# Optimization experiments

Measured on AMD Instinct MI355X. Metric: run time of the kernel, lower is better.

## Reference

```python
import jax, jax.numpy as jnp
import numpy as np

N, E, F_IN, EDGE_DIM, H, C, NUM_RELS = 20000, 160000, 64, 8, 4, 128, 4


def setup_inputs() -> dict:
    key = jax.random.key(0)
    ks = jax.random.split(key, 20)
    def rn(k, shape, s=0.05):
        return jax.random.normal(k, shape, jnp.float32) * s
    return {
        "x": rn(ks[0], (N, F_IN), 1.0),
        "edge_index": jax.random.randint(ks[1], (2, E), 0, N, dtype=jnp.int32),
        "edge_features": rn(ks[2], (E, EDGE_DIM), 1.0),
        "W1": rn(ks[3], (F_IN, H * C)), "a_src1": rn(ks[4], (H, C)), "a_dst1": rn(ks[5], (H, C)),
        "We1": rn(ks[6], (EDGE_DIM, H * C)), "a_e1": rn(ks[7], (H, C)), "b1": jnp.zeros((H * C,), jnp.float32),
        "W2": rn(ks[8], (H * C, H * C)), "a_src2": rn(ks[9], (H, C)), "a_dst2": rn(ks[10], (H, C)),
        "We2": rn(ks[11], (EDGE_DIM, H * C)), "a_e2": rn(ks[12], (H, C)), "b2": jnp.zeros((H * C,), jnp.float32),
        "Wd1": rn(ks[13], (2 * H * C, 256)), "bd1": jnp.zeros((256,), jnp.float32),
        "Wd2": rn(ks[14], (256, NUM_RELS)), "bd2": jnp.zeros((NUM_RELS,), jnp.float32),
    }


def _add_self_loops(ei, ea, n):
    # PyG add_self_loops with fill_value='mean': self-loop edge_attr is the
    # mean of incoming edge_attr per destination node (0 if no incoming edges).
    dst = ei[1]
    s = jax.ops.segment_sum(ea, dst, num_segments=n)
    cnt = jax.ops.segment_sum(jnp.ones((ea.shape[0], 1), ea.dtype), dst, num_segments=n)
    mean = s / jnp.maximum(cnt, 1.0)
    loop = jnp.arange(n, dtype=ei.dtype)
    ei2 = jnp.concatenate([ei, jnp.stack([loop, loop])], axis=1)
    ea2 = jnp.concatenate([ea, mean], axis=0)
    return ei2, ea2


def _gat_conv(x, ei, ea, W, a_s, a_d, We, a_e, b, n):
    ei, ea = _add_self_loops(ei, ea, n)
    src, dst = ei[0], ei[1]
    xp = (x @ W).reshape(n, H, C)                      # [N,H,C]
    alpha_s = jnp.einsum('nhc,hc->nh', xp, a_s)        # [N,H]
    alpha_d = jnp.einsum('nhc,hc->nh', xp, a_d)        # [N,H]
    ep = (ea @ We).reshape(-1, H, C)                   # [E',H,C]
    alpha_e = jnp.einsum('ehc,hc->eh', ep, a_e)        # [E',H]
    alpha = alpha_s[src] + alpha_d[dst] + alpha_e
    alpha = jax.nn.leaky_relu(alpha, 0.2)
    # segment softmax over edges sharing a destination node
    m = jax.ops.segment_max(alpha, dst, num_segments=n)
    ex = jnp.exp(alpha - m[dst])
    den = jax.ops.segment_sum(ex, dst, num_segments=n)
    w = ex / den[dst]                                   # [E',H]
    out = jax.ops.segment_sum(xp[src] * w[..., None], dst, num_segments=n)  # [N,H,C]
    return out.reshape(n, H * C) + b


def reference(x, edge_index, edge_features, W1, a_src1, a_dst1, We1, a_e1, b1,
              W2, a_src2, a_dst2, We2, a_e2, b2, Wd1, bd1, Wd2, bd2):
    n = x.shape[0]
    z = jax.nn.elu(_gat_conv(x, edge_index, edge_features, W1, a_src1, a_dst1, We1, a_e1, b1, n))
    z = jax.nn.elu(_gat_conv(z, edge_index, edge_features, W2, a_src2, a_dst2, We2, a_e2, b2, n))
    src, dst = edge_index[0], edge_index[1]
    rel = jnp.concatenate([z[src], z[dst]], axis=1)     # [E, 2*512]
    h = rel @ Wd1 + bd1                                 # dropout is identity at inference
    return jax.nn.sigmoid(h @ Wd2 + bd2)
```

## Files before the change

kernel.cpp:

```cpp
#include <hip/hip_runtime.h>
#include <hip/hip_bf16.h>
#include <math.h>

#define N_NODES 20000
#define N_EDGES 160000
#define FIN 64
#define EDGE_DIM 8
#define H_HEADS 4
#define C_CH 128
#define HC 512
#define NUM_RELS 4
#define E_TOT (N_EDGES + N_NODES)
#define E_PAD 320256

typedef __bf16 bf16x8 __attribute__((ext_vector_type(8)));
typedef __bf16 bf16x4 __attribute__((ext_vector_type(4)));
typedef float f32x4 __attribute__((ext_vector_type(4)));
typedef unsigned short u16x8 __attribute__((ext_vector_type(8)));

#define NZ4 ((N_NODES + E_PAD) / 4)
#define NM4 (E_PAD / 4)
__global__ void k_fill(int4* __restrict__ zbase, int4* __restrict__ mbase) {
    int tid = blockIdx.x * 256 + threadIdx.x;
    if (tid < NZ4) {
        zbase[tid] = make_int4(0, 0, 0, 0);
    } else if (tid < NZ4 + NM4) {
        mbase[tid - NZ4] = make_int4(-1, -1, -1, -1);
    }
}

#define NX4 (N_NODES * FIN / 4)
#define W1T (HC * FIN)
#define W2T (HC * HC)
#define NCVTB ((NX4 + W1T + W2T) / 256)
__global__ void k_prep_all(const float* __restrict__ x, __bf16* __restrict__ xb,
                           const float* __restrict__ W1, __bf16* __restrict__ Wt1,
                           const float* __restrict__ W2, __bf16* __restrict__ Wt2,
                           const float* __restrict__ We1, const float* __restrict__ ae1,
                           const float* __restrict__ We2, const float* __restrict__ ae2,
                           float* __restrict__ q1, float* __restrict__ q2,
                           const float* __restrict__ Wd1, const float* __restrict__ Wd2,
                           const float* __restrict__ bd1, const float* __restrict__ bd2,
                           float* __restrict__ M, float* __restrict__ cvec,
                           const float* __restrict__ as1, const float* __restrict__ ad1,
                           float* __restrict__ w1as, float* __restrict__ w1ad) {
    int bid = blockIdx.x;
    if (bid < NCVTB) {
        int tid = bid * 256 + threadIdx.x;
        if (tid < NX4) {
            float4 v = *(const float4*)(x + (size_t)tid * 4);
            __bf16 o[4] = {(__bf16)v.x, (__bf16)v.y, (__bf16)v.z, (__bf16)v.w};
            *(ushort2*)(xb + (size_t)tid * 4) = *(ushort2*)o;
            *(ushort2*)(xb + (size_t)tid * 4 + 2) = *(ushort2*)(o + 2);
        } else if (tid < NX4 + W1T) {
            int t = tid - NX4;
            int n = t / FIN, k = t % FIN;
            Wt1[n * FIN + k] = (__bf16)W1[(size_t)k * HC + n];
        } else {
            int t = tid - NX4 - W1T;
            int n = t >> 9, k = t & 511;
            Wt2[n * HC + k] = (__bf16)W2[(size_t)k * HC + n];
        }
        return;
    }
    int pb = bid - NCVTB;
    if (pb == 16) {
        int t = threadIdx.x;
        if (t >= 64) return;
        const float* We = (t < 32) ? We1 : We2;
        const float* ae = (t < 32) ? ae1 : ae2;
        float* q = (t < 32) ? q1 : q2;
        int i = t & 31, h = i >> 3, d = i & 7;
        float s = 0.f;
        for (int c = 0; c < 128; ++c) s += We[d * 512 + h * 128 + c] * ae[h * 128 + c];
        q[i] = s;
    } else if (pb == 17 || pb == 18) {
        int t = threadIdx.x;
        int h = t >> 6, k = t & 63;
        const float* av = (pb == 17) ? as1 : ad1;
        float* outp = (pb == 17) ? w1as : w1ad;
        float s = 0.f;
        for (int c = 0; c < 128; ++c) s += W1[(size_t)k * HC + h * 128 + c] * av[h * 128 + c];
        outp[h * 64 + k] = s;
    } else {
        int tid = pb * 256 + threadIdx.x;
        int i = tid >> 2, r = tid & 3;
        float s = 0.f;
        for (int k = 0; k < 256; ++k) s += Wd1[i * 256 + k] * Wd2[k * 4 + r];
        M[tid] = s;
        if (tid < 4) {
            float c = 0.f;
            for (int k = 0; k < 256; ++k) c += bd1[k] * Wd2[k * 4 + tid];
            cvec[tid] = c + bd2[tid];
        }
    }
}

#define LDP 40
__global__ __launch_bounds__(256)
void k_gemm_bf16(const __bf16* __restrict__ A, const __bf16* __restrict__ Bt,
                 __bf16* __restrict__ Ch, int M, int K,
                 const float* __restrict__ a_s2, const float* __restrict__ a_d2,
                 float* __restrict__ as_, float* __restrict__ ad_) {
    __shared__ __bf16 As[128 * LDP];
    __shared__ __bf16 Bs[128 * LDP];

    int nwg = gridDim.x;
    int f = blockIdx.x;
    int q = nwg >> 3, r = nwg & 7;
    int xcd = f & 7, idx = f >> 3;
    int wg = (xcd < r ? xcd * (q + 1) : r * (q + 1) + (xcd - r) * q) + idx;
    int by = wg >> 2, bx = wg & 3;
    int br = by * 128, bc = bx * 128;

    const int t = threadIdx.x;
    const int lane = t & 63;
    const int wid = t >> 6;
    const int wr = wid >> 1, wc = wid & 1;
    const int l15 = lane & 15, lkg = lane >> 4;

    const int srow = t >> 1, shalf = (t & 1) * 16;
    const int agr = br + srow;
    const __bf16* Ap = A + (size_t)agr * K + shalf;
    const __bf16* Bp = Bt + (size_t)(bc + srow) * K + shalf;

    f32x4 acc[4][4] = {};

    for (int k0 = 0; k0 < K; k0 += 32) {
        u16x8 av0 = {}, av1 = {};
        if (agr < M) {
            av0 = *(const u16x8*)(Ap + k0);
            av1 = *(const u16x8*)(Ap + k0 + 8);
        }
        u16x8 bv0 = *(const u16x8*)(Bp + k0);
        u16x8 bv1 = *(const u16x8*)(Bp + k0 + 8);
        *(u16x8*)(As + srow * LDP + shalf) = av0;
        *(u16x8*)(As + srow * LDP + shalf + 8) = av1;
        *(u16x8*)(Bs + srow * LDP + shalf) = bv0;
        *(u16x8*)(Bs + srow * LDP + shalf + 8) = bv1;
        __syncthreads();

        bf16x8 a[4], b[4];
        #pragma unroll
        for (int m = 0; m < 4; ++m)
            a[m] = *(const bf16x8*)(As + (wr * 64 + m * 16 + l15) * LDP + lkg * 8);
        #pragma unroll
        for (int n = 0; n < 4; ++n)
            b[n] = *(const bf16x8*)(Bs + (wc * 64 + n * 16 + l15) * LDP + lkg * 8);
        #pragma unroll
        for (int m = 0; m < 4; ++m)
            #pragma unroll
            for (int n = 0; n < 4; ++n)
                acc[m][n] = __builtin_amdgcn_mfma_f32_16x16x32_bf16(a[m], b[n], acc[m][n], 0, 0, 0);
        __syncthreads();
    }

    #pragma unroll
    for (int m = 0; m < 4; ++m) {
        int rbase = br + wr * 64 + m * 16 + lkg * 4;
        #pragma unroll
        for (int n = 0; n < 4; ++n) {
            int lcol = wc * 64 + n * 16 + l15;
            #pragma unroll
            for (int rg = 0; rg < 4; ++rg) {
                int gr = rbase + rg;
                if (gr < M)
                    Ch[((size_t)bx * N_NODES + gr) * 128 + lcol] = (__bf16)acc[m][n][rg];
            }
        }
    }

    float as_w[4], ad_w[4];
    #pragma unroll
    for (int n = 0; n < 4; ++n) {
        int col = wc * 64 + n * 16 + l15;
        as_w[n] = a_s2[bx * 128 + col];
        ad_w[n] = a_d2[bx * 128 + col];
    }
    float* sred = (float*)As;
    #pragma unroll
    for (int m = 0; m < 4; ++m) {
        #pragma unroll
        for (int rg = 0; rg < 4; ++rg) {
            float s = 0.f, d = 0.f;
            #pragma unroll
            for (int n = 0; n < 4; ++n) {
                float c = acc[m][n][rg];
                s += c * as_w[n];
                d += c * ad_w[n];
            }
            #pragma unroll
            for (int off = 1; off <= 8; off <<= 1) {
                s += __shfl_xor(s, off);
                d += __shfl_xor(d, off);
            }
            if (l15 == 0) {
                int lrow = wr * 64 + m * 16 + lkg * 4 + rg;
                sred[lrow * 2 + wc] = s;
                sred[256 + lrow * 2 + wc] = d;
            }
        }
    }
    __syncthreads();
    if (t < 128) {
        int gr = br + t;
        if (gr < M) {
            as_[gr * 4 + bx] = sred[t * 2] + sred[t * 2 + 1];
            ad_[gr * 4 + bx] = sred[256 + t * 2] + sred[256 + t * 2 + 1];
        }
    }
}

__global__ __launch_bounds__(256)
void k_gemm_head(const __bf16* __restrict__ aggb, const __bf16* __restrict__ Wt1,
                 const float* __restrict__ b1, __bf16* __restrict__ z1b, int M) {
    __shared__ __bf16 As[128 * LDP];
    __shared__ __bf16 Bs[128 * LDP];
    const int h = blockIdx.x;
    const int br = blockIdx.y * 128;

    const int t = threadIdx.x;
    const int lane = t & 63;
    const int wid = t >> 6;
    const int wr = wid >> 1, wc = wid & 1;
    const int l15 = lane & 15, lkg = lane >> 4;

    const int srow = t >> 1, shalf = (t & 1) * 16;
    const int agr = br + srow;
    const __bf16* Ap = aggb + (size_t)agr * 256 + h * 64 + shalf;
    const __bf16* Bp = Wt1 + (size_t)(h * 128 + srow) * 64 + shalf;

    f32x4 acc[4][4] = {};

    #pragma unroll
    for (int k0 = 0; k0 < 64; k0 += 32) {
        u16x8 av0 = {}, av1 = {};
        if (agr < M) {
            av0 = *(const u16x8*)(Ap + k0);
            av1 = *(const u16x8*)(Ap + k0 + 8);
        }
        u16x8 bv0 = *(const u16x8*)(Bp + k0);
        u16x8 bv1 = *(const u16x8*)(Bp + k0 + 8);
        *(u16x8*)(As + srow * LDP + shalf) = av0;
        *(u16x8*)(As + srow * LDP + shalf + 8) = av1;
        *(u16x8*)(Bs + srow * LDP + shalf) = bv0;
        *(u16x8*)(Bs + srow * LDP + shalf + 8) = bv1;
        __syncthreads();

        bf16x8 a[4], b[4];
        #pragma unroll
        for (int m = 0; m < 4; ++m)
            a[m] = *(const bf16x8*)(As + (wr * 64 + m * 16 + l15) * LDP + lkg * 8);
        #pragma unroll
        for (int n = 0; n < 4; ++n)
            b[n] = *(const bf16x8*)(Bs + (wc * 64 + n * 16 + l15) * LDP + lkg * 8);
        #pragma unroll
        for (int m = 0; m < 4; ++m)
            #pragma unroll
            for (int n = 0; n < 4; ++n)
                acc[m][n] = __builtin_amdgcn_mfma_f32_16x16x32_bf16(a[m], b[n], acc[m][n], 0, 0, 0);
        __syncthreads();
    }

    #pragma unroll
    for (int m = 0; m < 4; ++m) {
        int rbase = br + wr * 64 + m * 16 + lkg * 4;
        #pragma unroll
        for (int n = 0; n < 4; ++n) {
            int gcol = h * 128 + wc * 64 + n * 16 + l15;
            float bias = b1[gcol];
            #pragma unroll
            for (int rg = 0; rg < 4; ++rg) {
                int gr = rbase + rg;
                if (gr < M) {
                    float v = acc[m][n][rg] + bias;
                    v = (v > 0.f) ? v : expm1f(v);
                    z1b[(size_t)gr * HC + gcol] = (__bf16)v;
                }
            }
        }
    }
}

__global__ void k_count(const int* __restrict__ ei, int* __restrict__ counts) {
    int e = blockIdx.x * 256 + threadIdx.x;
    if (e >= E_TOT) return;
    int dst = (e < N_EDGES) ? ei[N_EDGES + e] : (e - N_EDGES);
    atomicAdd(counts + dst, 1);
}

__global__ __launch_bounds__(1024)
void k_scan(const int* __restrict__ counts, int* __restrict__ row_start,
            int* __restrict__ nxt) {
    __shared__ int part[1024];
    int t = threadIdx.x;
    int base = t * 20;
    int pre[20];
    int s = 0;
    #pragma unroll
    for (int i = 0; i < 20; ++i) {
        int idx = base + i;
        int c = (idx < N_NODES) ? ((counts[idx] + 7) & ~7) : 0;
        pre[i] = s; s += c;
    }
    part[t] = s;
    __syncthreads();
    for (int off = 1; off < 1024; off <<= 1) {
        int v = (t >= off) ? part[t - off] : 0;
        __syncthreads();
        part[t] += v;
        __syncthreads();
    }
    int excl = (t == 0) ? 0 : part[t - 1];
    #pragma unroll
    for (int i = 0; i < 20; ++i) {
        int idx = base + i;
        if (idx < N_NODES) { int v = excl + pre[i]; row_start[idx] = v; nxt[idx] = v; }
    }
    if (t == 1023) row_start[N_NODES] = part[1023];
}

__global__ void k_scatter(const int* __restrict__ ei, int* __restrict__ nxt,
                          int* __restrict__ csr_src, int* __restrict__ csr_eid,
                          int* __restrict__ csr_dst) {
    int e = blockIdx.x * 256 + threadIdx.x;
    if (e >= E_TOT) return;
    int src, dst;
    if (e < N_EDGES) { src = ei[e]; dst = ei[N_EDGES + e]; }
    else             { src = dst = e - N_EDGES; }
    int pos = atomicAdd(nxt + dst, 1);
    csr_src[pos] = src;
    csr_eid[pos] = e;
    csr_dst[pos] = dst;
}

__global__ void k_mean_csr(const int* __restrict__ row_start, const int* __restrict__ csr_eid,
                           const float* __restrict__ ef, float* __restrict__ meanf) {
    int n = blockIdx.x * 32 + (threadIdx.x >> 3);
    int d = threadIdx.x & 7;
    if (n >= N_NODES) return;
    int rs = row_start[n], re = row_start[n + 1];
    float s = 0.f; int c = 0;
    for (int i = rs; i < re; ++i) {
        unsigned eid = (unsigned)csr_eid[i];
        if (eid < N_EDGES) { s += ef[(size_t)eid * 8 + d]; ++c; }
    }
    meanf[n * 8 + d] = s / fmaxf((float)c, 1.f);
}

__global__ __launch_bounds__(256)
void k_nodeab(const __bf16* __restrict__ xb, const float* __restrict__ w1as,
              const float* __restrict__ w1ad, float* __restrict__ as_,
              float* __restrict__ ad_) {
    int n = blockIdx.x * 4 + (threadIdx.x >> 6);
    int lane = threadIdx.x & 63;
    if (n >= N_NODES) return;
    float xv = (float)xb[(size_t)n * 64 + lane];
    float s[4], d[4];
    #pragma unroll
    for (int h = 0; h < 4; ++h) {
        s[h] = xv * w1as[h * 64 + lane];
        d[h] = xv * w1ad[h * 64 + lane];
    }
    #pragma unroll
    for (int off = 32; off; off >>= 1) {
        #pragma unroll
        for (int h = 0; h < 4; ++h) {
            s[h] += __shfl_xor(s[h], off);
            d[h] += __shfl_xor(d[h], off);
        }
    }
    if (lane == 0) {
        *(float4*)(as_ + n * 4) = make_float4(s[0], s[1], s[2], s[3]);
        *(float4*)(ad_ + n * 4) = make_float4(d[0], d[1], d[2], d[3]);
    }
}

__global__ void k_edge_ex(const int* __restrict__ csr_src, const int* __restrict__ csr_dst,
                          const int* __restrict__ csr_eid, const float* __restrict__ ef,
                          const float* __restrict__ meanf, const float* __restrict__ q,
                          const float* __restrict__ as_, const float* __restrict__ ad_,
                          float* __restrict__ wbuf) {
    int i = blockIdx.x * 256 + threadIdx.x;
    if (i >= E_PAD) return;
    int eid = csr_eid[i];
    if (eid == -1) {
        *(float4*)(wbuf + (size_t)i * 4) = make_float4(0.f, 0.f, 0.f, 0.f);
        return;
    }
    int src = csr_src[i], dst = csr_dst[i];
    const float* fe = (eid < N_EDGES) ? (ef + (size_t)eid * 8)
                                      : (meanf + (size_t)(eid - N_EDGES) * 8);
    float f[8];
    #pragma unroll
    for (int d = 0; d < 8; ++d) f[d] = fe[d];
    float4 asv = *(const float4*)(as_ + src * 4);
    float4 adv = *(const float4*)(ad_ + dst * 4);
    const float* asp = &asv.x;
    const float* adp = &adv.x;
    float4 o;
    float* op = &o.x;
    #pragma unroll
    for (int h = 0; h < 4; ++h) {
        float ae = 0.f;
        #pragma unroll
        for (int d = 0; d < 8; ++d) ae += f[d] * q[h * 8 + d];
        float a = asp[h] + adp[h] + ae;
        a = (a > 0.f) ? a : 0.2f * a;
        op[h] = expf(a);
    }
    *(float4*)(wbuf + (size_t)i * 4) = o;
}

__global__ __launch_bounds__(256)
void k_gather1(const int* __restrict__ row_start, const int* __restrict__ csr_src,
               const float* __restrict__ wbuf, const __bf16* __restrict__ xb,
               __bf16* __restrict__ aggb) {
    int wv = threadIdx.x >> 6;
    int n = blockIdx.x * 4 + wv;
    int lane = threadIdx.x & 63;
    if (n >= N_NODES) return;
    int rs = row_start[n], re = row_start[n + 1];
    float acc[4] = {};
    float den[4] = {};

    for (int i = rs; i < re; i += 8) {
        unsigned short xr[8];
        float4 wr[8];
        #pragma unroll
        for (int p = 0; p < 8; ++p) {
            int sp = csr_src[i + p];
            xr[p] = *(const unsigned short*)(xb + (size_t)sp * 64 + lane);
            wr[p] = *(const float4*)(wbuf + (size_t)(i + p) * 4);
        }
        __builtin_amdgcn_sched_barrier(0);
        #pragma unroll
        for (int p = 0; p < 8; ++p) {
            float xv = (float)*(const __bf16*)&xr[p];
            acc[0] += wr[p].x * xv; den[0] += wr[p].x;
            acc[1] += wr[p].y * xv; den[1] += wr[p].y;
            acc[2] += wr[p].z * xv; den[2] += wr[p].z;
            acc[3] += wr[p].w * xv; den[3] += wr[p].w;
        }
    }
    #pragma unroll
    for (int h = 0; h < 4; ++h)
        aggb[(size_t)n * 256 + h * 64 + lane] = (__bf16)(acc[h] / den[h]);
}

__global__ __launch_bounds__(256)
void k_gather2h(const int* __restrict__ row_start, const int* __restrict__ csr_src,
                const float* __restrict__ wbuf, const __bf16* __restrict__ xph,
                const float* __restrict__ b2, const float* __restrict__ Mm,
                float* __restrict__ Up, float* __restrict__ Vp) {
    int h = blockIdx.y;
    int wv = threadIdx.x >> 6;
    int n = blockIdx.x * 4 + wv;
    int lane = threadIdx.x & 63;
    if (n >= N_NODES) return;
    int rs = row_start[n], re = row_start[n + 1];
    const __bf16* xbase = xph + (size_t)h * N_NODES * 128 + lane * 2;
    float a0 = 0.f, a1 = 0.f, den = 0.f;

    int i = rs;
    for (; i + 16 <= re; i += 16) {
        unsigned xr[16];
        float wr[16];
        #pragma unroll
        for (int p = 0; p < 16; ++p) {
            int sp = csr_src[i + p];
            wr[p] = wbuf[(size_t)(i + p) * 4 + h];
            xr[p] = *(const unsigned*)(xbase + (size_t)sp * 128);
        }
        __builtin_amdgcn_sched_barrier(0);
        #pragma unroll
        for (int p = 0; p < 16; ++p) {
            __bf16 b0 = *(const __bf16*)&xr[p];
            __bf16 b1v = *((const __bf16*)&xr[p] + 1);
            den += wr[p];
            a0 += wr[p] * (float)b0;
            a1 += wr[p] * (float)b1v;
        }
    }
    for (; i < re; i += 8) {
        unsigned xr[8];
        float wr[8];
        #pragma unroll
        for (int p = 0; p < 8; ++p) {
            int sp = csr_src[i + p];
            wr[p] = wbuf[(size_t)(i + p) * 4 + h];
            xr[p] = *(const unsigned*)(xbase + (size_t)sp * 128);
        }
        __builtin_amdgcn_sched_barrier(0);
        #pragma unroll
        for (int p = 0; p < 8; ++p) {
            __bf16 b0 = *(const __bf16*)&xr[p];
            __bf16 b1v = *((const __bf16*)&xr[p] + 1);
            den += wr[p];
            a0 += wr[p] * (float)b0;
            a1 += wr[p] * (float)b1v;
        }
    }
    float inv = 1.f / den;
    float v0 = a0 * inv + b2[h * 128 + lane * 2];
    float v1 = a1 * inv + b2[h * 128 + lane * 2 + 1];
    v0 = (v0 > 0.f) ? v0 : expm1f(v0);
    v1 = (v1 > 0.f) ? v1 : expm1f(v1);

    const float* m0 = Mm + (h * 128 + lane * 2) * 4;
    const float* n0 = Mm + 2048 + (h * 128 + lane * 2) * 4;
    float up[4], vp[4];
    #pragma unroll
    for (int r = 0; r < 4; ++r) {
        up[r] = v0 * m0[r] + v1 * m0[4 + r];
        vp[r] = v0 * n0[r] + v1 * n0[4 + r];
    }
    #pragma unroll
    for (int off = 32; off; off >>= 1) {
        #pragma unroll
        for (int r = 0; r < 4; ++r) {
            up[r] += __shfl_xor(up[r], off);
            vp[r] += __shfl_xor(vp[r], off);
        }
    }
    if (lane == 0) {
        *(float4*)(Up + ((size_t)h * N_NODES + n) * 4) = make_float4(up[0], up[1], up[2], up[3]);
        *(float4*)(Vp + ((size_t)h * N_NODES + n) * 4) = make_float4(vp[0], vp[1], vp[2], vp[3]);
    }
}

__global__ void k_edge_out(const int* __restrict__ ei, const float* __restrict__ Up,
                           const float* __restrict__ Vp, const float* __restrict__ cvec,
                           float* __restrict__ out) {
    int e = blockIdx.x * 256 + threadIdx.x;
    if (e >= N_EDGES) return;
    int s = ei[e], d = ei[N_EDGES + e];
    float4 u = make_float4(0.f, 0.f, 0.f, 0.f);
    float4 v = make_float4(0.f, 0.f, 0.f, 0.f);
    #pragma unroll
    for (int h = 0; h < 4; ++h) {
        float4 uh = *(const float4*)(Up + ((size_t)h * N_NODES + s) * 4);
        float4 vh = *(const float4*)(Vp + ((size_t)h * N_NODES + d) * 4);
        u.x += uh.x; u.y += uh.y; u.z += uh.z; u.w += uh.w;
        v.x += vh.x; v.y += vh.y; v.z += vh.z; v.w += vh.w;
    }
    float4 c = *(const float4*)cvec;
    float4 o;
    o.x = 1.f / (1.f + expf(-(u.x + v.x + c.x)));
    o.y = 1.f / (1.f + expf(-(u.y + v.y + c.y)));
    o.z = 1.f / (1.f + expf(-(u.z + v.z + c.z)));
    o.w = 1.f / (1.f + expf(-(u.w + v.w + c.w)));
    *(float4*)(out + (size_t)e * 4) = o;
}

extern "C" void kernel_launch(void* const* d_in, const int* in_sizes, int n_in,
                              void* d_out, int out_size, void* d_ws, size_t ws_size,
                              hipStream_t stream) {
    (void)in_sizes; (void)n_in; (void)out_size; (void)ws_size;
    const float* x      = (const float*)d_in[0];
    const int*   ei     = (const int*)d_in[1];
    const float* ef     = (const float*)d_in[2];
    const float* W1     = (const float*)d_in[3];
    const float* a_src1 = (const float*)d_in[4];
    const float* a_dst1 = (const float*)d_in[5];
    const float* We1    = (const float*)d_in[6];
    const float* a_e1   = (const float*)d_in[7];
    const float* b1     = (const float*)d_in[8];
    const float* W2     = (const float*)d_in[9];
    const float* a_src2 = (const float*)d_in[10];
    const float* a_dst2 = (const float*)d_in[11];
    const float* We2    = (const float*)d_in[12];
    const float* a_e2   = (const float*)d_in[13];
    const float* b2     = (const float*)d_in[14];
    const float* Wd1    = (const float*)d_in[15];
    const float* bd1    = (const float*)d_in[16];
    const float* Wd2    = (const float*)d_in[17];
    const float* bd2    = (const float*)d_in[18];
    float* out = (float*)d_out;

    float* wbuf   = (float*)d_ws;
    float* as_    = wbuf + (size_t)E_PAD * 4;
    float* ad_    = as_ + N_NODES * 4;
    float* meanf  = ad_ + N_NODES * 4;
    float* q1     = meanf + N_NODES * 8;
    float* q2     = q1 + 32;
    float* w1as   = q2 + 32;
    float* w1ad   = w1as + 256;
    float* Mm     = w1ad + 256;
    float* cv     = Mm + 4096;
    float* Up     = cv + 4;
    float* Vp     = Up + (size_t)N_NODES * 16;
    int* row_start = (int*)(Vp + (size_t)N_NODES * 16);
    int* nxt       = row_start + 20004;
    int* counts    = nxt + N_NODES;
    int* csr_src   = counts + N_NODES;
    int* csr_eid   = csr_src + E_PAD;
    int* csr_dst   = csr_eid + E_PAD;
    __bf16* xb   = (__bf16*)(csr_dst + E_PAD);
    __bf16* aggb = xb + (size_t)N_NODES * FIN;
    __bf16* z1b  = aggb + (size_t)N_NODES * 256;
    __bf16* xph2 = z1b + (size_t)N_NODES * HC;
    __bf16* Wt1  = xph2 + (size_t)N_NODES * HC;
    __bf16* Wt2  = Wt1 + HC * FIN;

    k_fill<<<(NZ4 + NM4 + 255) / 256, 256, 0, stream>>>((int4*)counts, (int4*)csr_eid);
    k_count<<<(E_TOT + 255) / 256, 256, 0, stream>>>(ei, counts);
    k_scan<<<1, 1024, 0, stream>>>(counts, row_start, nxt);
    k_scatter<<<(E_TOT + 255) / 256, 256, 0, stream>>>(ei, nxt, csr_src, csr_eid, csr_dst);
    k_mean_csr<<<(N_NODES + 31) / 32, 256, 0, stream>>>(row_start, csr_eid, ef, meanf);
    k_prep_all<<<NCVTB + 19, 256, 0, stream>>>(x, xb, W1, Wt1, W2, Wt2,
                                               We1, a_e1, We2, a_e2, q1, q2,
                                               Wd1, Wd2, bd1, bd2, Mm, cv,
                                               a_src1, a_dst1, w1as, w1ad);

    const int nblk = (N_NODES + 3) / 4;
    const int nby = (N_NODES + 127) / 128;

    k_nodeab<<<nblk, 256, 0, stream>>>(xb, w1as, w1ad, as_, ad_);
    k_edge_ex<<<(E_PAD + 255) / 256, 256, 0, stream>>>(csr_src, csr_dst, csr_eid, ef, meanf,
                                                       q1, as_, ad_, wbuf);
    k_gather1<<<nblk, 256, 0, stream>>>(row_start, csr_src, wbuf, xb, aggb);
    k_gemm_head<<<dim3(4, nby), 256, 0, stream>>>(aggb, Wt1, b1, z1b, N_NODES);

    k_gemm_bf16<<<nby * 4, 256, 0, stream>>>(z1b, Wt2, xph2, N_NODES, HC,
                                             a_src2, a_dst2, as_, ad_);
    k_edge_ex<<<(E_PAD + 255) / 256, 256, 0, stream>>>(csr_src, csr_dst, csr_eid, ef, meanf,
                                                       q2, as_, ad_, wbuf);
    k_gather2h<<<dim3(nblk, 4), 256, 0, stream>>>(row_start, csr_src, wbuf, xph2, b2,
                                                  Mm, Up, Vp);

    k_edge_out<<<(N_EDGES + 255) / 256, 256, 0, stream>>>(ei, Up, Vp, cv, out);
}
```

Before: 235.1 us.

## Tile weight transposes through shared memory and precompute softmax denominators with atomics

The weight-transpose part of the prep kernel now stages 64x64 tiles in padded shared memory, so both the W1/W2 reads and the transposed bf16 writes are coalesced instead of strided. Separately, the softmax denominators are accumulated in the edge kernel with per-destination atomicAdds into zeroed buffers, which the gather kernels then read instead of summing weights themselves. This removes a few adds per edge in the gathers but adds four float atomics per edge. The zero-fill region is also enlarged to clear the new denominator buffers, and atomic summation order makes the results nondeterministic.

```diff
diff --git a/kernel.cpp b/kernel.cpp
--- a/kernel.cpp
+++ b/kernel.cpp
@@ -18,7 +18,7 @@
 typedef float f32x4 __attribute__((ext_vector_type(4)));
 typedef unsigned short u16x8 __attribute__((ext_vector_type(8)));
 
-#define NZ4 ((N_NODES + E_PAD) / 4)
+#define NZ4 ((9 * N_NODES + E_PAD) / 4)
 #define NM4 (E_PAD / 4)
 __global__ void k_fill(int4* __restrict__ zbase, int4* __restrict__ mbase) {
     int tid = blockIdx.x * 256 + threadIdx.x;
@@ -30,9 +30,10 @@
 }
 
 #define NX4 (N_NODES * FIN / 4)
-#define W1T (HC * FIN)
-#define W2T (HC * HC)
-#define NCVTB ((NX4 + W1T + W2T) / 256)
+#define XB  (NX4 / 256)
+#define W1B 8
+#define W2B 64
+#define PREPB 19
 __global__ void k_prep_all(const float* __restrict__ x, __bf16* __restrict__ xb,
                            const float* __restrict__ W1, __bf16* __restrict__ Wt1,
                            const float* __restrict__ W2, __bf16* __restrict__ Wt2,
@@ -44,28 +45,52 @@
                            float* __restrict__ M, float* __restrict__ cvec,
                            const float* __restrict__ as1, const float* __restrict__ ad1,
                            float* __restrict__ w1as, float* __restrict__ w1ad) {
+    __shared__ float tile[64][65];
     int bid = blockIdx.x;
-    if (bid < NCVTB) {
-        int tid = bid * 256 + threadIdx.x;
-        if (tid < NX4) {
-            float4 v = *(const float4*)(x + (size_t)tid * 4);
-            __bf16 o[4] = {(__bf16)v.x, (__bf16)v.y, (__bf16)v.z, (__bf16)v.w};
-            *(ushort2*)(xb + (size_t)tid * 4) = *(ushort2*)o;
-            *(ushort2*)(xb + (size_t)tid * 4 + 2) = *(ushort2*)(o + 2);
-        } else if (tid < NX4 + W1T) {
-            int t = tid - NX4;
-            int n = t / FIN, k = t % FIN;
-            Wt1[n * FIN + k] = (__bf16)W1[(size_t)k * HC + n];
-        } else {
-            int t = tid - NX4 - W1T;
-            int n = t >> 9, k = t & 511;
-            Wt2[n * HC + k] = (__bf16)W2[(size_t)k * HC + n];
-        }
+    int t = threadIdx.x;
+    if (bid < XB) {
+        int tid = bid * 256 + t;
+        float4 v = *(const float4*)(x + (size_t)tid * 4);
+        __bf16 o[4] = {(__bf16)v.x, (__bf16)v.y, (__bf16)v.z, (__bf16)v.w};
+        *(ushort2*)(xb + (size_t)tid * 4) = *(ushort2*)o;
+        *(ushort2*)(xb + (size_t)tid * 4 + 2) = *(ushort2*)(o + 2);
         return;
     }
-    int pb = bid - NCVTB;
+    if (bid < XB + W1B) {
+        int tn = bid - XB;
+        int rr = t >> 6, cc = t & 63;
+        #pragma unroll
+        for (int i = 0; i < 16; ++i) {
+            int row = rr * 16 + i;
+            tile[row][cc] = W1[(size_t)row * HC + tn * 64 + cc];
+        }
+        __syncthreads();
+        #pragma unroll
+        for (int i = 0; i < 16; ++i) {
+            int row = rr * 16 + i;
+            Wt1[(size_t)(tn * 64 + row) * 64 + cc] = (__bf16)tile[cc][row];
+        }
+        return;
+    }
+    if (bid < XB + W1B + W2B) {
+        int p2 = bid - XB - W1B;
+        int tk = p2 >> 3, tn = p2 & 7;
+        int rr = t >> 6, cc = t & 63;
+        #pragma unroll
+        for (int i = 0; i < 16; ++i) {
+            int row = rr * 16 + i;
+            tile[row][cc] = W2[(size_t)(tk * 64 + row) * HC + tn * 64 + cc];
+        }
+        __syncthreads();
+        #pragma unroll
+        for (int i = 0; i < 16; ++i) {
+            int row = rr * 16 + i;
+            Wt2[(size_t)(tn * 64 + row) * HC + tk * 64 + cc] = (__bf16)tile[cc][row];
+        }
+        return;
+    }
+    int pb = bid - XB - W1B - W2B;
     if (pb == 16) {
-        int t = threadIdx.x;
         if (t >= 64) return;
         const float* We = (t < 32) ? We1 : We2;
         const float* ae = (t < 32) ? ae1 : ae2;
@@ -75,7 +100,6 @@
         for (int c = 0; c < 128; ++c) s += We[d * 512 + h * 128 + c] * ae[h * 128 + c];
         q[i] = s;
     } else if (pb == 17 || pb == 18) {
-        int t = threadIdx.x;
         int h = t >> 6, k = t & 63;
         const float* av = (pb == 17) ? as1 : ad1;
         float* outp = (pb == 17) ? w1as : w1ad;
@@ -83,7 +107,7 @@
         for (int c = 0; c < 128; ++c) s += W1[(size_t)k * HC + h * 128 + c] * av[h * 128 + c];
         outp[h * 64 + k] = s;
     } else {
-        int tid = pb * 256 + threadIdx.x;
+        int tid = pb * 256 + t;
         int i = tid >> 2, r = tid & 3;
         float s = 0.f;
         for (int k = 0; k < 256; ++k) s += Wd1[i * 256 + k] * Wd2[k * 4 + r];
@@ -380,7 +404,7 @@
                           const int* __restrict__ csr_eid, const float* __restrict__ ef,
                           const float* __restrict__ meanf, const float* __restrict__ q,
                           const float* __restrict__ as_, const float* __restrict__ ad_,
-                          float* __restrict__ wbuf) {
+                          float* __restrict__ wbuf, float* __restrict__ den) {
     int i = blockIdx.x * 256 + threadIdx.x;
     if (i >= E_PAD) return;
     int eid = csr_eid[i];
@@ -408,6 +432,7 @@
         float a = asp[h] + adp[h] + ae;
         a = (a > 0.f) ? a : 0.2f * a;
         op[h] = expf(a);
+        atomicAdd(den + dst * 4 + h, op[h]);
     }
     *(float4*)(wbuf + (size_t)i * 4) = o;
 }
@@ -415,14 +440,13 @@
 __global__ __launch_bounds__(256)
 void k_gather1(const int* __restrict__ row_start, const int* __restrict__ csr_src,
                const float* __restrict__ wbuf, const __bf16* __restrict__ xb,
-               __bf16* __restrict__ aggb) {
+               const float* __restrict__ den1, __bf16* __restrict__ aggb) {
     int wv = threadIdx.x >> 6;
     int n = blockIdx.x * 4 + wv;
     int lane = threadIdx.x & 63;
     if (n >= N_NODES) return;
     int rs = row_start[n], re = row_start[n + 1];
     float acc[4] = {};
-    float den[4] = {};
 
     for (int i = rs; i < re; i += 8) {
         unsigned short xr[8];
@@ -437,21 +461,24 @@
         #pragma unroll
         for (int p = 0; p < 8; ++p) {
             float xv = (float)*(const __bf16*)&xr[p];
-            acc[0] += wr[p].x * xv; den[0] += wr[p].x;
-            acc[1] += wr[p].y * xv; den[1] += wr[p].y;
-            acc[2] += wr[p].z * xv; den[2] += wr[p].z;
-            acc[3] += wr[p].w * xv; den[3] += wr[p].w;
-        }
-    }
+            acc[0] += wr[p].x * xv;
+            acc[1] += wr[p].y * xv;
+            acc[2] += wr[p].z * xv;
+            acc[3] += wr[p].w * xv;
+        }
+    }
+    float4 dv = *(const float4*)(den1 + n * 4);
+    const float* dvp = &dv.x;
     #pragma unroll
     for (int h = 0; h < 4; ++h)
-        aggb[(size_t)n * 256 + h * 64 + lane] = (__bf16)(acc[h] / den[h]);
+        aggb[(size_t)n * 256 + h * 64 + lane] = (__bf16)(acc[h] / dvp[h]);
 }
 
 __global__ __launch_bounds__(256)
 void k_gather2h(const int* __restrict__ row_start, const int* __restrict__ csr_src,
                 const float* __restrict__ wbuf, const __bf16* __restrict__ xph,
                 const float* __restrict__ b2, const float* __restrict__ Mm,
+                const float* __restrict__ den2,
                 float* __restrict__ Up, float* __restrict__ Vp) {
     int h = blockIdx.y;
     int wv = threadIdx.x >> 6;
@@ -460,7 +487,7 @@
     if (n >= N_NODES) return;
     int rs = row_start[n], re = row_start[n + 1];
     const __bf16* xbase = xph + (size_t)h * N_NODES * 128 + lane * 2;
-    float a0 = 0.f, a1 = 0.f, den = 0.f;
+    float a0 = 0.f, a1 = 0.f;
 
     int i = rs;
     for (; i + 16 <= re; i += 16) {
@@ -477,7 +504,6 @@
         for (int p = 0; p < 16; ++p) {
             __bf16 b0 = *(const __bf16*)&xr[p];
             __bf16 b1v = *((const __bf16*)&xr[p] + 1);
-            den += wr[p];
             a0 += wr[p] * (float)b0;
             a1 += wr[p] * (float)b1v;
         }
@@ -496,12 +522,11 @@
         for (int p = 0; p < 8; ++p) {
             __bf16 b0 = *(const __bf16*)&xr[p];
             __bf16 b1v = *((const __bf16*)&xr[p] + 1);
-            den += wr[p];
             a0 += wr[p] * (float)b0;
             a1 += wr[p] * (float)b1v;
         }
     }
-    float inv = 1.f / den;
+    float inv = 1.f / den2[n * 4 + h];
     float v0 = a0 * inv + b2[h * 128 + lane * 2];
     float v1 = a1 * inv + b2[h * 128 + lane * 2 + 1];
     v0 = (v0 > 0.f) ? v0 : expm1f(v0);
@@ -594,7 +619,9 @@
     int* nxt       = row_start + 20004;
     int* counts    = nxt + N_NODES;
     int* csr_src   = counts + N_NODES;
-    int* csr_eid   = csr_src + E_PAD;
+    float* den1    = (float*)(csr_src + E_PAD);
+    float* den2    = den1 + N_NODES * 4;
+    int* csr_eid   = (int*)(den2 + N_NODES * 4);
     int* csr_dst   = csr_eid + E_PAD;
     __bf16* xb   = (__bf16*)(csr_dst + E_PAD);
     __bf16* aggb = xb + (size_t)N_NODES * FIN;
@@ -608,26 +635,26 @@
     k_scan<<<1, 1024, 0, stream>>>(counts, row_start, nxt);
     k_scatter<<<(E_TOT + 255) / 256, 256, 0, stream>>>(ei, nxt, csr_src, csr_eid, csr_dst);
     k_mean_csr<<<(N_NODES + 31) / 32, 256, 0, stream>>>(row_start, csr_eid, ef, meanf);
-    k_prep_all<<<NCVTB + 19, 256, 0, stream>>>(x, xb, W1, Wt1, W2, Wt2,
-                                               We1, a_e1, We2, a_e2, q1, q2,
-                                               Wd1, Wd2, bd1, bd2, Mm, cv,
-                                               a_src1, a_dst1, w1as, w1ad);
+    k_prep_all<<<XB + W1B + W2B + PREPB, 256, 0, stream>>>(x, xb, W1, Wt1, W2, Wt2,
+                                                           We1, a_e1, We2, a_e2, q1, q2,
+                                                           Wd1, Wd2, bd1, bd2, Mm, cv,
+                                                           a_src1, a_dst1, w1as, w1ad);
 
     const int nblk = (N_NODES + 3) / 4;
     const int nby = (N_NODES + 127) / 128;
 
     k_nodeab<<<nblk, 256, 0, stream>>>(xb, w1as, w1ad, as_, ad_);
     k_edge_ex<<<(E_PAD + 255) / 256, 256, 0, stream>>>(csr_src, csr_dst, csr_eid, ef, meanf,
-                                                       q1, as_, ad_, wbuf);
-    k_gather1<<<nblk, 256, 0, stream>>>(row_start, csr_src, wbuf, xb, aggb);
+                                                       q1, as_, ad_, wbuf, den1);
+    k_gather1<<<nblk, 256, 0, stream>>>(row_start, csr_src, wbuf, xb, den1, aggb);
     k_gemm_head<<<dim3(4, nby), 256, 0, stream>>>(aggb, Wt1, b1, z1b, N_NODES);
 
     k_gemm_bf16<<<nby * 4, 256, 0, stream>>>(z1b, Wt2, xph2, N_NODES, HC,
                                              a_src2, a_dst2, as_, ad_);
     k_edge_ex<<<(E_PAD + 255) / 256, 256, 0, stream>>>(csr_src, csr_dst, csr_eid, ef, meanf,
-                                                       q2, as_, ad_, wbuf);
+                                                       q2, as_, ad_, wbuf, den2);
     k_gather2h<<<dim3(nblk, 4), 256, 0, stream>>>(row_start, csr_src, wbuf, xph2, b2,
-                                                  Mm, Up, Vp);
+                                                  Mm, den2, Up, Vp);
 
     k_edge_out<<<(N_EDGES + 255) / 256, 256, 0, stream>>>(ei, Up, Vp, cv, out);
 }
```

Result: slower. 318.0 us (+35.3%).
